# Kernel tuning notes

Measured on AMD Instinct MI355X. Metric: run time of the kernel, lower is better.

## Reference

```python
import jax, jax.numpy as jnp
import numpy as np

D_MODEL = 1024
NUM_HEADS = 16
DEPTH = D_MODEL // NUM_HEADS  # 64
BATCH, SEQ = 4, 2048


def setup_inputs() -> dict:
    key = jax.random.key(0)
    ks = jax.random.split(key, 9)
    s = 1.0 / np.sqrt(D_MODEL)
    x = jax.random.normal(ks[0], (BATCH, SEQ, D_MODEL), dtype=jnp.float32)
    # Per-head Dense weights stacked on a leading head axis [H, d_model, depth]
    Wq = jax.random.normal(ks[1], (NUM_HEADS, D_MODEL, DEPTH), dtype=jnp.float32) * s
    Wk = jax.random.normal(ks[2], (NUM_HEADS, D_MODEL, DEPTH), dtype=jnp.float32) * s
    Wv = jax.random.normal(ks[3], (NUM_HEADS, D_MODEL, DEPTH), dtype=jnp.float32) * s
    bq = jnp.zeros((NUM_HEADS, DEPTH), dtype=jnp.float32)
    bk = jnp.zeros((NUM_HEADS, DEPTH), dtype=jnp.float32)
    bv = jnp.zeros((NUM_HEADS, DEPTH), dtype=jnp.float32)
    Wo = jax.random.normal(ks[4], (D_MODEL, D_MODEL), dtype=jnp.float32) * s
    bo = jnp.zeros((D_MODEL,), dtype=jnp.float32)
    return {"x": x, "Wq": Wq, "bq": bq, "Wk": Wk, "bk": bk,
            "Wv": Wv, "bv": bv, "Wo": Wo, "bo": bo}


def reference(x, Wq, bq, Wk, bk, Wv, bv, Wo, bo):
    # Batched equivalent of the per-head loop: project, attend, concat heads.
    q = jnp.einsum('bsd,hde->bhse', x, Wq) + bq[:, None, :]  # [B,H,S,depth]
    k = jnp.einsum('bsd,hde->bhse', x, Wk) + bk[:, None, :]
    v = jnp.einsum('bsd,hde->bhse', x, Wv) + bv[:, None, :]
    scale = 1.0 / jnp.sqrt(jnp.asarray(DEPTH, dtype=x.dtype))
    scores = jnp.einsum('bhse,bhte->bhst', q, k) * scale      # [B,H,S,S]
    weights = jax.nn.softmax(scores, axis=-1)
    heads = jnp.einsum('bhst,bhte->bhse', weights, v)         # [B,H,S,depth]
    # concat head outputs along last axis in head order (tf.concat axis=-1)
    multi = jnp.transpose(heads, (0, 2, 1, 3)).reshape(x.shape[0], x.shape[1], D_MODEL)
    return multi @ Wo + bo
```

## Files before the change

### kernel.cpp

```cpp
#include <hip/hip_runtime.h>
#include <hip/hip_bf16.h>

#define BATCH 4
#define SEQ   2048
#define DM    1024
#define NH    16
#define DEPTH 64
#define ROWS  (BATCH*SEQ)
#define NQKV  (3*DM)
#define BH    (BATCH*NH)

typedef __attribute__((ext_vector_type(8))) short bf16x8;
typedef __attribute__((ext_vector_type(4))) float f32x4;
typedef unsigned short u16;
typedef unsigned int   u32;

__device__ __forceinline__ u16 f2bf(float f) {
    union { float f; unsigned u; } v; v.f = f;
    unsigned r = v.u + 0x7fff + ((v.u >> 16) & 1);
    return (u16)(r >> 16);
}

__device__ __forceinline__ u32 pk2bf(float a, float b) {
#if __has_builtin(__builtin_amdgcn_cvt_pk_bf16_f32)
    typedef __attribute__((ext_vector_type(2))) __bf16 v2bf;
    union { v2bf v; u32 u; } u_;
    u_.v = __builtin_amdgcn_cvt_pk_bf16_f32(a, b);
    return u_.u;
#else
    return (u32)f2bf(a) | ((u32)f2bf(b) << 16);
#endif
}

__device__ __forceinline__ void g2l16(void* lds, const void* g) {
    __builtin_amdgcn_global_load_lds((const __attribute__((address_space(1))) void*)g,
                                     (__attribute__((address_space(3))) void*)lds, 16, 0, 0);
}

__device__ __forceinline__ bf16x8 frag8(const u16* tile, int row, int gl) {
    return *(const bf16x8*)(tile + row * 64 + ((gl ^ (row & 7)) * 8));
}

__global__ __launch_bounds__(256) void k_cvt_x(const float* __restrict__ x, u16* __restrict__ xb) {
    int i = (blockIdx.x * 256 + threadIdx.x) * 4;
    float4 v = *(const float4*)(x + i);
    ushort4 o; o.x = f2bf(v.x); o.y = f2bf(v.y); o.z = f2bf(v.z); o.w = f2bf(v.w);
    *(ushort4*)(xb + i) = o;
}

__global__ __launch_bounds__(256) void k_build_wqkv(const float* __restrict__ Wq, const float* __restrict__ Wk,
                                                    const float* __restrict__ Wv, u16* __restrict__ BT) {
    int idx = blockIdx.x * 256 + threadIdx.x;
    int k = idx & 1023;
    int n = idx >> 10;
    int m = n >> 10;
    int h = (n >> 6) & 15;
    int e = n & 63;
    const float* W = (m == 0) ? Wq : (m == 1) ? Wk : Wv;
    BT[idx] = f2bf(W[(h * 1024 + k) * 64 + e]);
}

__global__ __launch_bounds__(256) void k_build_wot(const float* __restrict__ Wo, u16* __restrict__ WoT) {
    int idx = blockIdx.x * 256 + threadIdx.x;
    int k = idx & 1023, n = idx >> 10;
    WoT[idx] = f2bf(Wo[k * 1024 + n]);
}

__global__ __launch_bounds__(256) void k_gemm_qkv(const u16* __restrict__ A, const u16* __restrict__ BT,
                                                  const float* __restrict__ bq, const float* __restrict__ bk,
                                                  const float* __restrict__ bv,
                                                  u16* __restrict__ Q, u16* __restrict__ K, u16* __restrict__ VT) {
    __shared__ u16 Al[128 * 64];
    __shared__ u16 Bl[128 * 64];
    int tid = threadIdx.x;
    int wave = tid >> 6, lane = tid & 63, ln = lane & 15, quad = lane >> 4;
    int row0 = blockIdx.y * 128;
    int col0 = blockIdx.x * 128;
    int moff = (wave >> 1) * 64, noff = (wave & 1) * 64;
    f32x4 acc[4][4] = {};

    for (int k0 = 0; k0 < 1024; k0 += 64) {
        for (int l = 0; l < 4; ++l) {
            int idx = tid + l * 256, r = idx >> 3, gs = ((idx & 7) ^ (r & 7)) * 8;
            g2l16(&Al[idx * 8], A  + (row0 + r) * 1024 + k0 + gs);
            g2l16(&Bl[idx * 8], BT + (col0 + r) * 1024 + k0 + gs);
        }
        __syncthreads();
        for (int kk = 0; kk < 2; ++kk) {
            bf16x8 a[4], b[4];
            for (int i = 0; i < 4; ++i) a[i] = frag8(Al, moff + i * 16 + ln, kk * 4 + quad);
            for (int j = 0; j < 4; ++j) b[j] = frag8(Bl, noff + j * 16 + ln, kk * 4 + quad);
            for (int i = 0; i < 4; ++i)
                for (int j = 0; j < 4; ++j)
                    acc[i][j] = __builtin_amdgcn_mfma_f32_16x16x32_bf16(a[i], b[j], acc[i][j], 0, 0, 0);
        }
        __syncthreads();
    }

    const float QSCALE = 0.125f * 1.4426950408889634f;
    for (int j = 0; j < 4; ++j) {
        int c = col0 + noff + j * 16 + ln;
        int m = c >> 10, h = (c >> 6) & 15, e = c & 63;
        const float* bias = (m == 0) ? bq : (m == 1) ? bk : bv;
        float bval = bias[h * 64 + e];
        for (int i = 0; i < 4; ++i) {
            for (int r = 0; r < 4; ++r) {
                int rowg = row0 + moff + i * 16 + quad * 4 + r;
                int b_ = rowg >> 11, s = rowg & 2047;
                int bh = b_ * 16 + h;
                float v = acc[i][j][r] + bval;
                if (m == 0)      Q[(bh * 2048 + s) * 64 + e] = f2bf(v * QSCALE);
                else if (m == 1) K[(bh * 2048 + s) * 64 + e] = f2bf(v);
                else             VT[(bh * 64 + e) * 2048 + s] = f2bf(v);
            }
        }
    }
}

__global__ __launch_bounds__(256) void k_attn(const u16* __restrict__ Q, const u16* __restrict__ K,
                                              const u16* __restrict__ VT, u16* __restrict__ A2) {
    __shared__ u16 Ql[128 * 64];
    __shared__ u16 Kl[64 * 64];
    __shared__ u16 Vl[64 * 64];
    int tid = threadIdx.x;
    int wave = tid >> 6, lane = tid & 63, ln = lane & 15, quad = lane >> 4;
    int bh = blockIdx.y;
    int m0 = blockIdx.x * 128;
    const u16* Qb = Q + (size_t)bh * 2048 * 64;
    const u16* Kb = K + (size_t)bh * 2048 * 64;
    const u16* Vb = VT + (size_t)bh * 64 * 2048;

    for (int l = 0; l < 4; ++l) {
        int idx = tid + l * 256, r = idx >> 3, gs = ((idx & 7) ^ (r & 7)) * 8;
        g2l16(&Ql[idx * 8], Qb + (m0 + r) * 64 + gs);
    }
    __syncthreads();
    bf16x8 qb[2][2];
    for (int s = 0; s < 2; ++s)
        for (int kk = 0; kk < 2; ++kk)
            qb[s][kk] = frag8(Ql, wave * 32 + s * 16 + ln, kk * 4 + quad);

    int rA = tid >> 3,          gA = (((tid) & 7) ^ (rA & 7)) * 8;
    int idxB = tid + 256;
    int rB = idxB >> 3,         gB = ((idxB & 7) ^ (rB & 7)) * 8;
    const u16* kgA = Kb + rA * 64 + gA;
    const u16* kgB = Kb + rB * 64 + gB;
    const u16* vgA = Vb + rA * 2048 + gA;
    const u16* vgB = Vb + rB * 2048 + gB;

    float lrun[2] = {0.f, 0.f};
    f32x4 oacc[2][4] = {};

    for (int t = 0; t < 32; ++t) {
        g2l16(&Kl[tid * 8],  kgA + t * 4096);
        g2l16(&Kl[idxB * 8], kgB + t * 4096);
        g2l16(&Vl[tid * 8],  vgA + t * 64);
        g2l16(&Vl[idxB * 8], vgB + t * 64);
        __syncthreads();

        f32x4 sc[2][4] = {};
        for (int kk = 0; kk < 2; ++kk) {
            bf16x8 kf[4];
            for (int j = 0; j < 4; ++j) kf[j] = frag8(Kl, j * 16 + ln, kk * 4 + quad);
            for (int s = 0; s < 2; ++s)
                for (int j = 0; j < 4; ++j)
                    sc[s][j] = __builtin_amdgcn_mfma_f32_16x16x32_bf16(kf[j], qb[s][kk], sc[s][j], 0, 0, 0);
        }

        for (int s = 0; s < 2; ++s) {
            int prow = wave * 32 + s * 16 + ln;
            char* pbase = (char*)Ql + prow * 128 + (quad & 1) * 8;
            float sum = 0.f;
            for (int j = 0; j < 4; ++j) {
                float p0 = __builtin_amdgcn_exp2f(sc[s][j][0]);
                float p1 = __builtin_amdgcn_exp2f(sc[s][j][1]);
                float p2 = __builtin_amdgcn_exp2f(sc[s][j][2]);
                float p3 = __builtin_amdgcn_exp2f(sc[s][j][3]);
                sum += (p0 + p1) + (p2 + p3);
                uint2 w; w.x = pk2bf(p0, p1); w.y = pk2bf(p2, p3);
                int pg = (j * 2 + (quad >> 1)) ^ (ln & 7);
                *(uint2*)(pbase + pg * 16) = w;
            }
            lrun[s] += sum;
        }

        for (int kk = 0; kk < 2; ++kk) {
            bf16x8 ap0 = frag8(Ql, wave * 32 + ln,      kk * 4 + quad);
            bf16x8 ap1 = frag8(Ql, wave * 32 + 16 + ln, kk * 4 + quad);
            for (int et = 0; et < 4; ++et) {
                bf16x8 bv_ = frag8(Vl, et * 16 + ln, kk * 4 + quad);
                oacc[0][et] = __builtin_amdgcn_mfma_f32_16x16x32_bf16(ap0, bv_, oacc[0][et], 0, 0, 0);
                oacc[1][et] = __builtin_amdgcn_mfma_f32_16x16x32_bf16(ap1, bv_, oacc[1][et], 0, 0, 0);
            }
        }
        __syncthreads();
    }

    int b_ = bh >> 4, h = bh & 15;
    for (int s = 0; s < 2; ++s) {
        float l = lrun[s];
        l += __shfl_xor(l, 16);
        l += __shfl_xor(l, 32);
        float inv = 1.0f / l;
        for (int r = 0; r < 4; ++r) {
            float ir = __shfl(inv, quad * 4 + r, 16);
            int rowg = b_ * 2048 + m0 + wave * 32 + s * 16 + quad * 4 + r;
            for (int et = 0; et < 4; ++et)
                A2[rowg * 1024 + h * 64 + et * 16 + ln] = f2bf(oacc[s][et][r] * ir);
        }
    }
}

__global__ __launch_bounds__(256) void k_gemm_out(const u16* __restrict__ A, const u16* __restrict__ BT,
                                                  const float* __restrict__ bo, float* __restrict__ out) {
    __shared__ u16 Al[128 * 64];
    __shared__ u16 Bl[128 * 64];
    int tid = threadIdx.x;
    int wave = tid >> 6, lane = tid & 63, ln = lane & 15, quad = lane >> 4;
    int row0 = blockIdx.y * 128;
    int col0 = blockIdx.x * 128;
    int moff = (wave >> 1) * 64, noff = (wave & 1) * 64;
    f32x4 acc[4][4] = {};

    for (int k0 = 0; k0 < 1024; k0 += 64) {
        for (int l = 0; l < 4; ++l) {
            int idx = tid + l * 256, r = idx >> 3, gs = ((idx & 7) ^ (r & 7)) * 8;
            g2l16(&Al[idx * 8], A  + (row0 + r) * 1024 + k0 + gs);
            g2l16(&Bl[idx * 8], BT + (col0 + r) * 1024 + k0 + gs);
        }
        __syncthreads();
        for (int kk = 0; kk < 2; ++kk) {
            bf16x8 a[4], b[4];
            for (int i = 0; i < 4; ++i) a[i] = frag8(Al, moff + i * 16 + ln, kk * 4 + quad);
            for (int j = 0; j < 4; ++j) b[j] = frag8(Bl, noff + j * 16 + ln, kk * 4 + quad);
            for (int i = 0; i < 4; ++i)
                for (int j = 0; j < 4; ++j)
                    acc[i][j] = __builtin_amdgcn_mfma_f32_16x16x32_bf16(a[i], b[j], acc[i][j], 0, 0, 0);
        }
        __syncthreads();
    }

    for (int j = 0; j < 4; ++j) {
        int c = col0 + noff + j * 16 + ln;
        float bias = bo[c];
        for (int i = 0; i < 4; ++i)
            for (int r = 0; r < 4; ++r) {
                int rowg = row0 + moff + i * 16 + quad * 4 + r;
                out[rowg * 1024 + c] = acc[i][j][r] + bias;
            }
    }
}

extern "C" void kernel_launch(void* const* d_in, const int* in_sizes, int n_in,
                              void* d_out, int out_size, void* d_ws, size_t ws_size,
                              hipStream_t stream) {
    const float* x  = (const float*)d_in[0];
    const float* Wq = (const float*)d_in[1];
    const float* bq = (const float*)d_in[2];
    const float* Wk = (const float*)d_in[3];
    const float* bk = (const float*)d_in[4];
    const float* Wv = (const float*)d_in[5];
    const float* bv = (const float*)d_in[6];
    const float* Wo = (const float*)d_in[7];
    const float* bo = (const float*)d_in[8];
    float* out = (float*)d_out;

    char* ws = (char*)d_ws;
    u16* xb    = (u16*)ws; ws += (size_t)ROWS * DM * 2;
    u16* WqkvT = (u16*)ws; ws += (size_t)NQKV * DM * 2;
    u16* WoT   = (u16*)ws; ws += (size_t)DM * DM * 2;
    u16* Qb    = (u16*)ws; ws += (size_t)BH * SEQ * DEPTH * 2;
    u16* Kb    = (u16*)ws; ws += (size_t)BH * SEQ * DEPTH * 2;
    u16* VTb   = (u16*)ws; ws += (size_t)BH * SEQ * DEPTH * 2;
    u16* A2    = (u16*)ws; ws += (size_t)ROWS * DM * 2;

    k_cvt_x     <<<dim3(ROWS * DM / 1024), dim3(256), 0, stream>>>(x, xb);
    k_build_wqkv<<<dim3(NQKV * DM / 256),  dim3(256), 0, stream>>>(Wq, Wk, Wv, WqkvT);
    k_build_wot <<<dim3(DM * DM / 256),    dim3(256), 0, stream>>>(Wo, WoT);
    k_gemm_qkv  <<<dim3(24, 64), dim3(256), 0, stream>>>(xb, WqkvT, bq, bk, bv, Qb, Kb, VTb);
    k_attn      <<<dim3(16, 64), dim3(256), 0, stream>>>(Qb, Kb, VTb, A2);
    k_gemm_out  <<<dim3(8, 64),  dim3(256), 0, stream>>>(A2, WoT, bo, out);
}
```

Before: 337.4 us.

## Fuse prep kernels, split V projection into transposed GEMM, prefetch K/V in attention

Merges the three conversion kernels into one launch and transposes weights through LDS tiles, replacing the strided scalar gather. The V projection becomes its own GEMM computing V^T directly (weights as A, activations as B), so the VT stores are coalesced along the sequence instead of strided. In attention, the row sum moves onto an MFMA against a ones vector, and each K/V tile load is issued right after the previous compute, with an extra barrier per iteration. The risk is the added sync and a very small grid (8 row tiles) for the V GEMM.

```diff
diff --git a/kernel.cpp b/kernel.cpp
--- a/kernel.cpp
+++ b/kernel.cpp
@@ -41,35 +41,51 @@
     return *(const bf16x8*)(tile + row * 64 + ((gl ^ (row & 7)) * 8));
 }
 
-__global__ __launch_bounds__(256) void k_cvt_x(const float* __restrict__ x, u16* __restrict__ xb) {
-    int i = (blockIdx.x * 256 + threadIdx.x) * 4;
-    float4 v = *(const float4*)(x + i);
-    ushort4 o; o.x = f2bf(v.x); o.y = f2bf(v.y); o.z = f2bf(v.z); o.w = f2bf(v.w);
-    *(ushort4*)(xb + i) = o;
-}
-
-__global__ __launch_bounds__(256) void k_build_wqkv(const float* __restrict__ Wq, const float* __restrict__ Wk,
-                                                    const float* __restrict__ Wv, u16* __restrict__ BT) {
-    int idx = blockIdx.x * 256 + threadIdx.x;
-    int k = idx & 1023;
-    int n = idx >> 10;
-    int m = n >> 10;
-    int h = (n >> 6) & 15;
-    int e = n & 63;
-    const float* W = (m == 0) ? Wq : (m == 1) ? Wk : Wv;
-    BT[idx] = f2bf(W[(h * 1024 + k) * 64 + e]);
-}
-
-__global__ __launch_bounds__(256) void k_build_wot(const float* __restrict__ Wo, u16* __restrict__ WoT) {
-    int idx = blockIdx.x * 256 + threadIdx.x;
-    int k = idx & 1023, n = idx >> 10;
-    WoT[idx] = f2bf(Wo[k * 1024 + n]);
-}
-
-__global__ __launch_bounds__(256) void k_gemm_qkv(const u16* __restrict__ A, const u16* __restrict__ BT,
-                                                  const float* __restrict__ bq, const float* __restrict__ bk,
-                                                  const float* __restrict__ bv,
-                                                  u16* __restrict__ Q, u16* __restrict__ K, u16* __restrict__ VT) {
+__global__ __launch_bounds__(256) void k_prep(const float* __restrict__ x,
+                                              const float* __restrict__ Wq, const float* __restrict__ Wk,
+                                              const float* __restrict__ Wv, const float* __restrict__ Wo,
+                                              u16* __restrict__ xb, u16* __restrict__ BT, u16* __restrict__ WoT) {
+    __shared__ u16 T[64][65];
+    int tid = threadIdx.x;
+    int bx = blockIdx.x;
+    if (bx < 2048) {
+        int i = bx * 4096 + tid * 4;
+        for (int l = 0; l < 4; ++l) {
+            float4 v = *(const float4*)(x + i + l * 1024);
+            ushort4 o; o.x = f2bf(v.x); o.y = f2bf(v.y); o.z = f2bf(v.z); o.w = f2bf(v.w);
+            *(ushort4*)(xb + i + l * 1024) = o;
+        }
+        return;
+    }
+    if (bx < 2816) {
+        int q = bx - 2048;
+        int kt = q & 15, mh = q >> 4, m = mh >> 4, h = mh & 15;
+        const float* W = (m == 0) ? Wq : (m == 1) ? Wk : Wv;
+        const float* src = W + ((size_t)h * 1024 + kt * 64) * 64;
+        int e = tid & 63, r0 = tid >> 6;
+        for (int i = 0; i < 16; ++i) { int r = i * 4 + r0; T[r][e] = f2bf(src[r * 64 + e]); }
+        __syncthreads();
+        int kk = tid & 63, e0 = tid >> 6;
+        u16* dst = BT + ((size_t)m * 1024 + h * 64) * 1024 + kt * 64;
+        for (int i = 0; i < 16; ++i) { int ee = i * 4 + e0; dst[ee * 1024 + kk] = T[kk][ee]; }
+        return;
+    }
+    {
+        int q = bx - 2816;
+        int kt = q & 15, nt = q >> 4;
+        const float* src = Wo + (size_t)kt * 64 * 1024 + nt * 64;
+        int c = tid & 63, r0 = tid >> 6;
+        for (int i = 0; i < 16; ++i) { int r = i * 4 + r0; T[r][c] = f2bf(src[r * 1024 + c]); }
+        __syncthreads();
+        int kk = tid & 63, e0 = tid >> 6;
+        u16* dst = WoT + (size_t)nt * 64 * 1024 + kt * 64;
+        for (int i = 0; i < 16; ++i) { int ee = i * 4 + e0; dst[ee * 1024 + kk] = T[kk][ee]; }
+    }
+}
+
+__global__ __launch_bounds__(256) void k_gemm_qk(const u16* __restrict__ A, const u16* __restrict__ BT,
+                                                 const float* __restrict__ bq, const float* __restrict__ bk,
+                                                 u16* __restrict__ Q, u16* __restrict__ K) {
     __shared__ u16 Al[128 * 64];
     __shared__ u16 Bl[128 * 64];
     int tid = threadIdx.x;
@@ -101,7 +117,7 @@
     for (int j = 0; j < 4; ++j) {
         int c = col0 + noff + j * 16 + ln;
         int m = c >> 10, h = (c >> 6) & 15, e = c & 63;
-        const float* bias = (m == 0) ? bq : (m == 1) ? bk : bv;
+        const float* bias = (m == 0) ? bq : bk;
         float bval = bias[h * 64 + e];
         for (int i = 0; i < 4; ++i) {
             for (int r = 0; r < 4; ++r) {
@@ -109,9 +125,50 @@
                 int b_ = rowg >> 11, s = rowg & 2047;
                 int bh = b_ * 16 + h;
                 float v = acc[i][j][r] + bval;
-                if (m == 0)      Q[(bh * 2048 + s) * 64 + e] = f2bf(v * QSCALE);
-                else if (m == 1) K[(bh * 2048 + s) * 64 + e] = f2bf(v);
-                else             VT[(bh * 64 + e) * 2048 + s] = f2bf(v);
+                if (m == 0) Q[(bh * 2048 + s) * 64 + e] = f2bf(v * QSCALE);
+                else        K[(bh * 2048 + s) * 64 + e] = f2bf(v);
+            }
+        }
+    }
+}
+
+__global__ __launch_bounds__(256) void k_gemm_vt(const u16* __restrict__ A, const u16* __restrict__ BT,
+                                                 const float* __restrict__ bv, u16* __restrict__ VT) {
+    __shared__ u16 Al[128 * 64];
+    __shared__ u16 Bl[128 * 64];
+    int tid = threadIdx.x;
+    int wave = tid >> 6, lane = tid & 63, ln = lane & 15, quad = lane >> 4;
+    int row0 = blockIdx.y * 128;
+    int col0 = blockIdx.x * 128;
+    int moff = (wave >> 1) * 64, noff = (wave & 1) * 64;
+    f32x4 acc[4][4] = {};
+
+    for (int k0 = 0; k0 < 1024; k0 += 64) {
+        for (int l = 0; l < 4; ++l) {
+            int idx = tid + l * 256, r = idx >> 3, gs = ((idx & 7) ^ (r & 7)) * 8;
+            g2l16(&Al[idx * 8], A  + (row0 + r) * 1024 + k0 + gs);
+            g2l16(&Bl[idx * 8], BT + (col0 + r) * 1024 + k0 + gs);
+        }
+        __syncthreads();
+        for (int kk = 0; kk < 2; ++kk) {
+            bf16x8 a[4], b[4];
+            for (int i = 0; i < 4; ++i) a[i] = frag8(Al, moff + i * 16 + ln, kk * 4 + quad);
+            for (int j = 0; j < 4; ++j) b[j] = frag8(Bl, noff + j * 16 + ln, kk * 4 + quad);
+            for (int i = 0; i < 4; ++i)
+                for (int j = 0; j < 4; ++j)
+                    acc[i][j] = __builtin_amdgcn_mfma_f32_16x16x32_bf16(a[i], b[j], acc[i][j], 0, 0, 0);
+        }
+        __syncthreads();
+    }
+
+    for (int j = 0; j < 4; ++j) {
+        int c = col0 + noff + j * 16 + ln;
+        int b_ = c >> 11, s = c & 2047;
+        for (int i = 0; i < 4; ++i) {
+            for (int r = 0; r < 4; ++r) {
+                int ii = row0 + moff + i * 16 + quad * 4 + r;
+                float v = acc[i][j][r] + bv[ii];
+                VT[((size_t)b_ * 1024 + ii) * 2048 + s] = f2bf(v);
             }
         }
     }
@@ -130,34 +187,35 @@
     const u16* Kb = K + (size_t)bh * 2048 * 64;
     const u16* Vb = VT + (size_t)bh * 64 * 2048;
 
+    int rA = tid >> 3,  gA = ((tid & 7) ^ (rA & 7)) * 8;
+    int idxB = tid + 256;
+    int rB = idxB >> 3, gB = ((idxB & 7) ^ (rB & 7)) * 8;
+    const u16* kgA = Kb + rA * 64 + gA;
+    const u16* kgB = Kb + rB * 64 + gB;
+    const u16* vgA = Vb + rA * 2048 + gA;
+    const u16* vgB = Vb + rB * 2048 + gB;
+
     for (int l = 0; l < 4; ++l) {
         int idx = tid + l * 256, r = idx >> 3, gs = ((idx & 7) ^ (r & 7)) * 8;
         g2l16(&Ql[idx * 8], Qb + (m0 + r) * 64 + gs);
     }
+    g2l16(&Kl[tid * 8],  kgA);
+    g2l16(&Kl[idxB * 8], kgB);
+    g2l16(&Vl[tid * 8],  vgA);
+    g2l16(&Vl[idxB * 8], vgB);
     __syncthreads();
     bf16x8 qb[2][2];
     for (int s = 0; s < 2; ++s)
         for (int kk = 0; kk < 2; ++kk)
             qb[s][kk] = frag8(Ql, wave * 32 + s * 16 + ln, kk * 4 + quad);
 
-    int rA = tid >> 3,          gA = (((tid) & 7) ^ (rA & 7)) * 8;
-    int idxB = tid + 256;
-    int rB = idxB >> 3,         gB = ((idxB & 7) ^ (rB & 7)) * 8;
-    const u16* kgA = Kb + rA * 64 + gA;
-    const u16* kgB = Kb + rB * 64 + gB;
-    const u16* vgA = Vb + rA * 2048 + gA;
-    const u16* vgB = Vb + rB * 2048 + gB;
-
-    float lrun[2] = {0.f, 0.f};
+    bf16x8 ones;
+    for (int i = 0; i < 8; ++i) ones[i] = (short)0x3F80;
+
     f32x4 oacc[2][4] = {};
+    f32x4 lacc[2] = {};
 
     for (int t = 0; t < 32; ++t) {
-        g2l16(&Kl[tid * 8],  kgA + t * 4096);
-        g2l16(&Kl[idxB * 8], kgB + t * 4096);
-        g2l16(&Vl[tid * 8],  vgA + t * 64);
-        g2l16(&Vl[idxB * 8], vgB + t * 64);
-        __syncthreads();
-
         f32x4 sc[2][4] = {};
         for (int kk = 0; kk < 2; ++kk) {
             bf16x8 kf[4];
@@ -170,18 +228,15 @@
         for (int s = 0; s < 2; ++s) {
             int prow = wave * 32 + s * 16 + ln;
             char* pbase = (char*)Ql + prow * 128 + (quad & 1) * 8;
-            float sum = 0.f;
             for (int j = 0; j < 4; ++j) {
                 float p0 = __builtin_amdgcn_exp2f(sc[s][j][0]);
                 float p1 = __builtin_amdgcn_exp2f(sc[s][j][1]);
                 float p2 = __builtin_amdgcn_exp2f(sc[s][j][2]);
                 float p3 = __builtin_amdgcn_exp2f(sc[s][j][3]);
-                sum += (p0 + p1) + (p2 + p3);
                 uint2 w; w.x = pk2bf(p0, p1); w.y = pk2bf(p2, p3);
                 int pg = (j * 2 + (quad >> 1)) ^ (ln & 7);
                 *(uint2*)(pbase + pg * 16) = w;
             }
-            lrun[s] += sum;
         }
 
         for (int kk = 0; kk < 2; ++kk) {
@@ -192,18 +247,23 @@
                 oacc[0][et] = __builtin_amdgcn_mfma_f32_16x16x32_bf16(ap0, bv_, oacc[0][et], 0, 0, 0);
                 oacc[1][et] = __builtin_amdgcn_mfma_f32_16x16x32_bf16(ap1, bv_, oacc[1][et], 0, 0, 0);
             }
+            lacc[0] = __builtin_amdgcn_mfma_f32_16x16x32_bf16(ap0, ones, lacc[0], 0, 0, 0);
+            lacc[1] = __builtin_amdgcn_mfma_f32_16x16x32_bf16(ap1, ones, lacc[1], 0, 0, 0);
+        }
+        __syncthreads();
+        if (t < 31) {
+            g2l16(&Kl[tid * 8],  kgA + (t + 1) * 4096);
+            g2l16(&Kl[idxB * 8], kgB + (t + 1) * 4096);
+            g2l16(&Vl[tid * 8],  vgA + (t + 1) * 64);
+            g2l16(&Vl[idxB * 8], vgB + (t + 1) * 64);
         }
         __syncthreads();
     }
 
     int b_ = bh >> 4, h = bh & 15;
     for (int s = 0; s < 2; ++s) {
-        float l = lrun[s];
-        l += __shfl_xor(l, 16);
-        l += __shfl_xor(l, 32);
-        float inv = 1.0f / l;
         for (int r = 0; r < 4; ++r) {
-            float ir = __shfl(inv, quad * 4 + r, 16);
+            float ir = 1.0f / lacc[s][r];
             int rowg = b_ * 2048 + m0 + wave * 32 + s * 16 + quad * 4 + r;
             for (int et = 0; et < 4; ++et)
                 A2[rowg * 1024 + h * 64 + et * 16 + ln] = f2bf(oacc[s][et][r] * ir);
@@ -274,10 +334,9 @@
     u16* VTb   = (u16*)ws; ws += (size_t)BH * SEQ * DEPTH * 2;
     u16* A2    = (u16*)ws; ws += (size_t)ROWS * DM * 2;
 
-    k_cvt_x     <<<dim3(ROWS * DM / 1024), dim3(256), 0, stream>>>(x, xb);
-    k_build_wqkv<<<dim3(NQKV * DM / 256),  dim3(256), 0, stream>>>(Wq, Wk, Wv, WqkvT);
-    k_build_wot <<<dim3(DM * DM / 256),    dim3(256), 0, stream>>>(Wo, WoT);
-    k_gemm_qkv  <<<dim3(24, 64), dim3(256), 0, stream>>>(xb, WqkvT, bq, bk, bv, Qb, Kb, VTb);
-    k_attn      <<<dim3(16, 64), dim3(256), 0, stream>>>(Qb, Kb, VTb, A2);
-    k_gemm_out  <<<dim3(8, 64),  dim3(256), 0, stream>>>(A2, WoT, bo, out);
-}
+    k_prep     <<<dim3(3072),   dim3(256), 0, stream>>>(x, Wq, Wk, Wv, Wo, xb, WqkvT, WoT);
+    k_gemm_qk  <<<dim3(16, 64), dim3(256), 0, stream>>>(xb, WqkvT, bq, bk, Qb, Kb);
+    k_gemm_vt  <<<dim3(64, 8),  dim3(256), 0, stream>>>(WqkvT + 2048 * 1024, xb, bv, VTb);
+    k_attn     <<<dim3(16, 64), dim3(256), 0, stream>>>(Qb, Kb, VTb, A2);
+    k_gemm_out <<<dim3(8, 64),  dim3(256), 0, stream>>>(A2, WoT, bo, out);
+}
```

Measured after the change: 301.2 us. -10.7%, faster.
